# Kernel tuning notes

Measured on AMD Instinct MI355X. Metric: run time of the kernel, lower is better.

The kernel has to match this reference:

```python
import jax, jax.numpy as jnp
import numpy as np

D_MODEL = 1024
NUM_HEADS = 16
D_HEAD = D_MODEL // NUM_HEADS


def setup_inputs() -> dict:
    key = jax.random.key(0)
    ks = jax.random.split(key, 7)
    B, S = 2, 2048
    scale = 1.0 / np.sqrt(D_MODEL)
    return {
        "x": jax.random.normal(ks[0], (B, S, D_MODEL), dtype=jnp.float32),
        "attn_weights": jnp.zeros((1,), dtype=jnp.float32),  # unused in original forward
        "Wq": jax.random.normal(ks[1], (D_MODEL, D_MODEL), dtype=jnp.float32) * scale,
        "Wk": jax.random.normal(ks[2], (D_MODEL, D_MODEL), dtype=jnp.float32) * scale,
        "Wv": jax.random.normal(ks[3], (D_MODEL, D_MODEL), dtype=jnp.float32) * scale,
        "Wp": jax.random.normal(ks[4], (D_MODEL, D_MODEL), dtype=jnp.float32) * scale,
        "bp": jnp.zeros((D_MODEL,), dtype=jnp.float32),
    }


def reference(x, attn_weights, Wq, Wk, Wv, Wp, bp):
    B, S, D = x.shape
    H, Dh = NUM_HEADS, D_HEAD
    # torch Linear: y = x @ W.T  (weights stored [out, in])
    q = (x @ Wq.T).reshape(B, S, H, Dh).transpose(0, 2, 1, 3)  # [B,H,S,Dh]
    k = (x @ Wk.T).reshape(B, S, H, Dh).transpose(0, 2, 1, 3)
    v = (x @ Wv.T).reshape(B, S, H, Dh).transpose(0, 2, 1, 3)
    # NOTE: original module applies NO 1/sqrt(d) scaling
    scores = jnp.einsum("bhqd,bhkd->bhqk", q, k)
    weights = jax.nn.softmax(scores, axis=-1)  # dropout is inference no-op
    out = jnp.einsum("bhqk,bhkd->bhqd", weights, v)
    out = out.transpose(0, 2, 1, 3).reshape(B, S, D)
    return out @ Wp.T + bp
```

## Files before the change

### kernel.cpp

```cpp
#include <hip/hip_runtime.h>
#include <hip/hip_bf16.h>

#define D_MODEL 1024
#define NUM_HEADS 16
#define D_HEAD 64
#define BATCH 2
#define SEQ 2048
#define TOKENS (BATCH * SEQ)

typedef __attribute__((ext_vector_type(8))) short bf16x8;
typedef __attribute__((ext_vector_type(4))) float f32x4;
typedef __attribute__((ext_vector_type(2))) unsigned int uint2v;

typedef __attribute__((address_space(1))) const unsigned int as1_uint;
typedef __attribute__((address_space(3))) unsigned int as3_uint;

#define LOG2E 1.44269504088896340736f

static __device__ __forceinline__ unsigned short f2bf(float f) {
    unsigned int u = __builtin_bit_cast(unsigned int, f);
    u += 0x7fffu + ((u >> 16) & 1u);
    return (unsigned short)(u >> 16);
}

static __device__ __forceinline__ unsigned int pk2bf(float a, float b) {
    __hip_bfloat162 h = __float22bfloat162_rn(float2{a, b});
    unsigned int u;
    __builtin_memcpy(&u, &h, 4);
    return u;
}

static __device__ __forceinline__ float fast_exp2(float x) {
    return __builtin_amdgcn_exp2f(x);
}

__global__ __launch_bounds__(256) void convert_bf16(
    const float* __restrict__ x,  const float* __restrict__ Wq,
    const float* __restrict__ Wk, const float* __restrict__ Wv,
    const float* __restrict__ Wp,
    unsigned short* __restrict__ xb,  unsigned short* __restrict__ Wqb,
    unsigned short* __restrict__ Wkb, unsigned short* __restrict__ Wvb,
    unsigned short* __restrict__ Wpb)
{
    int v = blockIdx.x * 256 + threadIdx.x;
    const float* s;
    unsigned short* d;
    int off;
    if (v < (1 << 20)) { s = x; d = xb; off = v; }
    else {
        int u = v - (1 << 20);
        int w = u >> 18;
        off = u & ((1 << 18) - 1);
        s = (w == 0) ? Wq : (w == 1) ? Wk : (w == 2) ? Wv : Wp;
        d = (w == 0) ? Wqb : (w == 1) ? Wkb : (w == 2) ? Wvb : Wpb;
    }
    float4 f = ((const float4*)s)[off];
    ushort4 o = { f2bf(f.x), f2bf(f.y), f2bf(f.z), f2bf(f.w) };
    ((ushort4*)d)[off] = o;
}

__global__ __launch_bounds__(512, 4) void qkv_gemm(
    const unsigned short* __restrict__ xb,
    const unsigned short* __restrict__ Wqb, const unsigned short* __restrict__ Wkb,
    const unsigned short* __restrict__ Wvb,
    unsigned short* __restrict__ Q, unsigned short* __restrict__ Kb,
    unsigned short* __restrict__ Vt)
{
    const int m0 = blockIdx.x * 128;
    const int n0 = blockIdx.y * 64;

    __shared__ __attribute__((aligned(16))) unsigned short sm[40960];

    const int t = threadIdx.x;
    const int wave = t >> 6, lane = t & 63;
    const int wm = (wave & 1) * 64, wn = (wave >> 1) * 16;
    const int l15 = lane & 15, quad = lane >> 4;
    const int sw = l15 & 7;

    const unsigned short* Wz[3] = { Wqb, Wkb, Wvb };

    f32x4 acc[3][4];
#pragma unroll
    for (int z = 0; z < 3; z++)
#pragma unroll
        for (int i = 0; i < 4; i++) acc[z][i] = (f32x4)0.f;

    auto stage = [&](int k0, int buf) {
#pragma unroll
        for (int i = 0; i < 2; i++) {
            int fbase = wave * 64 + i * 512;
            int f = fbase + lane;
            int row = f >> 3, cp = f & 7;
            int c = cp ^ (row & 7);
            __builtin_amdgcn_global_load_lds(
                (as1_uint*)&xb[(size_t)(m0 + row) * D_MODEL + k0 + c * 8],
                (as3_uint*)&sm[buf * 20480 + fbase * 8], 16, 0, 0);
        }
        {
            int row = t >> 3, cp = t & 7;
            int c = cp ^ (row & 7);
            int fbase = wave * 64;
#pragma unroll
            for (int z = 0; z < 3; z++)
                __builtin_amdgcn_global_load_lds(
                    (as1_uint*)&Wz[z][(size_t)(n0 + row) * D_MODEL + k0 + c * 8],
                    (as3_uint*)&sm[buf * 20480 + 8192 + z * 4096 + fbase * 8],
                    16, 0, 0);
        }
    };

    stage(0, 0);
    __syncthreads();

    int cur = 0;
    for (int k0 = 0; k0 < D_MODEL; k0 += 64) {
        if (k0 + 64 < D_MODEL) stage(k0 + 64, cur ^ 1);

        const unsigned short* lA = &sm[cur * 20480];
#pragma unroll
        for (int kk = 0; kk < 2; kk++) {
            const int cc = ((kk * 4 + quad) ^ sw) * 8;
            bf16x8 a[4];
#pragma unroll
            for (int mt = 0; mt < 4; mt++)
                a[mt] = *(const bf16x8*)&lA[(wm + mt * 16 + l15) * 64 + cc];
#pragma unroll
            for (int z = 0; z < 3; z++) {
                const unsigned short* lB = &sm[cur * 20480 + 8192 + z * 4096];
                bf16x8 b = *(const bf16x8*)&lB[(wn + l15) * 64 + cc];
#pragma unroll
                for (int mt = 0; mt < 4; mt++)
                    acc[z][mt] = __builtin_amdgcn_mfma_f32_16x16x32_bf16(
                        a[mt], b, acc[z][mt], 0, 0, 0);
            }
        }
        __syncthreads();
        cur ^= 1;
    }

#pragma unroll
    for (int mt = 0; mt < 4; mt++)
#pragma unroll
        for (int r = 0; r < 4; r++) {
            int row = m0 + wm + mt * 16 + quad * 4 + r;
            int col = n0 + wn + l15;
            Q[(size_t)row * D_MODEL + col]  = f2bf(acc[0][mt][r] * LOG2E);
            Kb[(size_t)row * D_MODEL + col] = f2bf(acc[1][mt][r]);
        }
    {
        const int b = m0 >> 11;
        const int srow = (m0 & 2047) + wm + quad * 4;
        const int h = n0 >> 6;
        const int dh = wn + l15;
#pragma unroll
        for (int mt = 0; mt < 4; mt++) {
            ushort4 pk = { f2bf(acc[2][mt][0]), f2bf(acc[2][mt][1]),
                           f2bf(acc[2][mt][2]), f2bf(acc[2][mt][3]) };
            *(ushort4*)&Vt[(size_t)((b * 16 + h) * 64 + dh) * SEQ + srow + mt * 16] = pk;
        }
    }
}

__global__ __launch_bounds__(512, 4) void attn(
    const unsigned short* __restrict__ Q, const unsigned short* __restrict__ K,
    const unsigned short* __restrict__ Vt, unsigned short* __restrict__ O)
{
    const int q0 = blockIdx.x * 128;
    const int bh = blockIdx.y;
    const int b = bh >> 4, h = bh & 15;
    const size_t base = (size_t)b * SEQ * D_MODEL + (size_t)h * D_HEAD;
    const size_t baseV = (size_t)bh * D_HEAD * SEQ;

    __shared__ __attribute__((aligned(16))) char smem[40960];
    unsigned short* lK0 = (unsigned short*)&smem[0];
    unsigned short* lV0 = (unsigned short*)&smem[16384];

    const int t = threadIdx.x;
    const int wave = t >> 6, lane = t & 63;
    const int l15 = lane & 15, quad = lane >> 4;
    const int wq = wave & 3;
    const int sh = wave >> 2;
    const int qw = q0 + wq * 32;
    const int sbase = sh * (SEQ / 2);

    unsigned short* lK  = lK0 + sh * 4096;
    unsigned short* lVt = lV0 + sh * 4096;

    bf16x8 ones;
#pragma unroll
    for (int i = 0; i < 8; i++) ones[i] = (short)0x3F80;

    bf16x8 bq[2][2];
#pragma unroll
    for (int mq = 0; mq < 2; mq++)
#pragma unroll
        for (int kk = 0; kk < 2; kk++)
            bq[mq][kk] = *(const bf16x8*)&Q[base +
                (size_t)(qw + mq * 16 + l15) * D_MODEL + kk * 32 + quad * 8];

    const int tl = t & 255;
    const int r0 = tl >> 3, c0 = tl & 7;
    const int cs = (c0 ^ (r0 & 7)) * 8;
    const unsigned short* gK0 = &K[base + (size_t)(sbase + r0) * D_MODEL + c0 * 8];
    const unsigned short* gK1 = &K[base + (size_t)(sbase + r0 + 32) * D_MODEL + c0 * 8];
    const unsigned short* gV0 = &Vt[baseV + (size_t)r0 * SEQ + sbase + c0 * 8];
    const unsigned short* gV1 = &Vt[baseV + (size_t)(r0 + 32) * SEQ + sbase + c0 * 8];

    const int sw = l15 & 7;

    f32x4 o_acc[2][4];
#pragma unroll
    for (int i = 0; i < 2; i++)
#pragma unroll
        for (int j = 0; j < 4; j++) o_acc[i][j] = (f32x4)0.f;
    f32x4 o_l[2];
#pragma unroll
    for (int i = 0; i < 2; i++) o_l[i] = (f32x4)0.f;

    uint4 rK0 = *(const uint4*)gK0;
    uint4 rK1 = *(const uint4*)gK1;
    uint4 rV0 = *(const uint4*)gV0;
    uint4 rV1 = *(const uint4*)gV1;

    for (int s0 = 0; s0 < SEQ / 2; s0 += 64) {
        __syncthreads();
        *(uint4*)&lK[r0 * 64 + cs]        = rK0;
        *(uint4*)&lK[(r0 + 32) * 64 + cs] = rK1;
        *(uint4*)&lVt[r0 * 64 + cs]        = rV0;
        *(uint4*)&lVt[(r0 + 32) * 64 + cs] = rV1;
        __syncthreads();

        int sn = (s0 + 64 < SEQ / 2) ? s0 + 64 : 0;
        rK0 = *(const uint4*)(gK0 + (size_t)sn * D_MODEL);
        rK1 = *(const uint4*)(gK1 + (size_t)sn * D_MODEL);
        rV0 = *(const uint4*)(gV0 + sn);
        rV1 = *(const uint4*)(gV1 + sn);

        f32x4 st[4][2];
#pragma unroll
        for (int mt = 0; mt < 4; mt++)
#pragma unroll
            for (int mq = 0; mq < 2; mq++) st[mt][mq] = (f32x4)0.f;
#pragma unroll
        for (int kk = 0; kk < 2; kk++) {
            const int cc = ((kk * 4 + quad) ^ sw) * 8;
#pragma unroll
            for (int mt = 0; mt < 4; mt++) {
                bf16x8 ak = *(const bf16x8*)&lK[(mt * 16 + l15) * 64 + cc];
#pragma unroll
                for (int mq = 0; mq < 2; mq++)
                    st[mt][mq] = __builtin_amdgcn_mfma_f32_16x16x32_bf16(
                        ak, bq[mq][kk], st[mt][mq], 0, 0, 0);
            }
        }

#pragma unroll
        for (int mq = 0; mq < 2; mq++)
#pragma unroll
            for (int mt = 0; mt < 4; mt++)
#pragma unroll
                for (int r = 0; r < 4; r++)
                    st[mt][mq][r] = fast_exp2(st[mt][mq][r]);

        bf16x8 pa[2][2];
#pragma unroll
        for (int mq = 0; mq < 2; mq++)
#pragma unroll
            for (int kk = 0; kk < 2; kk++) {
                unsigned int cw[4];
#pragma unroll
                for (int j = 0; j < 2; j++) {
                    unsigned int w0 = pk2bf(st[2 * kk][mq][2 * j],
                                            st[2 * kk][mq][2 * j + 1]);
                    unsigned int w1 = pk2bf(st[2 * kk + 1][mq][2 * j],
                                            st[2 * kk + 1][mq][2 * j + 1]);
                    uint2v uv = __builtin_amdgcn_permlane32_swap(w0, w1, false, false);
                    uint2v f  = __builtin_amdgcn_permlane16_swap(uv[0], uv[1], false, false);
                    cw[j]     = f[0];
                    cw[2 + j] = f[1];
                }
                union { unsigned int w[4]; bf16x8 v; } u;
                u.w[0] = cw[0]; u.w[1] = cw[1]; u.w[2] = cw[2]; u.w[3] = cw[3];
                pa[mq][kk] = u.v;
            }

#pragma unroll
        for (int kk = 0; kk < 2; kk++) {
            const int cc = ((kk * 4 + quad) ^ sw) * 8;
            bf16x8 bv[4];
#pragma unroll
            for (int nt = 0; nt < 4; nt++)
                bv[nt] = *(const bf16x8*)&lVt[(nt * 16 + l15) * 64 + cc];
#pragma unroll
            for (int mq = 0; mq < 2; mq++) {
#pragma unroll
                for (int nt = 0; nt < 4; nt++)
                    o_acc[mq][nt] = __builtin_amdgcn_mfma_f32_16x16x32_bf16(
                        pa[mq][kk], bv[nt], o_acc[mq][nt], 0, 0, 0);
                o_l[mq] = __builtin_amdgcn_mfma_f32_16x16x32_bf16(
                    pa[mq][kk], ones, o_l[mq], 0, 0, 0);
            }
        }
    }

    float* sO = (float*)&smem[0];
    float* sL = (float*)&smem[36864];
    __syncthreads();
    if (sh == 1) {
#pragma unroll
        for (int mq = 0; mq < 2; mq++) {
#pragma unroll
            for (int r = 0; r < 4; r++)
                sL[wq * 32 + mq * 16 + quad * 4 + r] = o_l[mq][r];
#pragma unroll
            for (int nt = 0; nt < 4; nt++)
#pragma unroll
                for (int r = 0; r < 4; r++)
                    sO[(wq * 32 + mq * 16 + quad * 4 + r) * 68 + nt * 16 + l15] =
                        o_acc[mq][nt][r];
        }
    }
    __syncthreads();
    if (sh == 0) {
#pragma unroll
        for (int mq = 0; mq < 2; mq++) {
            float inv[4];
#pragma unroll
            for (int r = 0; r < 4; r++)
                inv[r] = 1.f / (o_l[mq][r] + sL[wq * 32 + mq * 16 + quad * 4 + r]);
#pragma unroll
            for (int nt = 0; nt < 4; nt++)
#pragma unroll
                for (int r = 0; r < 4; r++) {
                    int row = qw + mq * 16 + quad * 4 + r;
                    float v = o_acc[mq][nt][r] +
                              sO[(wq * 32 + mq * 16 + quad * 4 + r) * 68 + nt * 16 + l15];
                    O[base + (size_t)row * D_MODEL + nt * 16 + l15] = f2bf(v * inv[r]);
                }
        }
    }
}

__global__ __launch_bounds__(512, 4) void proj_gemm(
    const unsigned short* __restrict__ A, const unsigned short* __restrict__ W,
    const float* __restrict__ bias, float* __restrict__ out)
{
    const int m0 = blockIdx.x * 128;
    const int n0 = blockIdx.y * 64;

    __shared__ __attribute__((aligned(16))) unsigned short sm[24576];

    const int t = threadIdx.x;
    const int wave = t >> 6, lane = t & 63;
    const int wm = (wave & 1) * 64, wn = (wave >> 1) * 16;
    const int l15 = lane & 15, quad = lane >> 4;
    const int sw = l15 & 7;

    f32x4 acc[4];
#pragma unroll
    for (int i = 0; i < 4; i++) acc[i] = (f32x4)0.f;

    auto stage = [&](int k0, int buf) {
#pragma unroll
        for (int i = 0; i < 2; i++) {
            int fbase = wave * 64 + i * 512;
            int f = fbase + lane;
            int row = f >> 3, cp = f & 7;
            int c = cp ^ (row & 7);
            __builtin_amdgcn_global_load_lds(
                (as1_uint*)&A[(size_t)(m0 + row) * D_MODEL + k0 + c * 8],
                (as3_uint*)&sm[buf * 12288 + fbase * 8], 16, 0, 0);
        }
        {
            int row = t >> 3, cp = t & 7;
            int c = cp ^ (row & 7);
            int fbase = wave * 64;
            __builtin_amdgcn_global_load_lds(
                (as1_uint*)&W[(size_t)(n0 + row) * D_MODEL + k0 + c * 8],
                (as3_uint*)&sm[buf * 12288 + 8192 + fbase * 8], 16, 0, 0);
        }
    };

    stage(0, 0);
    __syncthreads();

    int cur = 0;
    for (int k0 = 0; k0 < D_MODEL; k0 += 64) {
        if (k0 + 64 < D_MODEL) stage(k0 + 64, cur ^ 1);

        const unsigned short* lA = &sm[cur * 12288];
        const unsigned short* lB = &sm[cur * 12288 + 8192];
#pragma unroll
        for (int kk = 0; kk < 2; kk++) {
            const int cc = ((kk * 4 + quad) ^ sw) * 8;
            bf16x8 a[4];
#pragma unroll
            for (int mt = 0; mt < 4; mt++)
                a[mt] = *(const bf16x8*)&lA[(wm + mt * 16 + l15) * 64 + cc];
            bf16x8 b = *(const bf16x8*)&lB[(wn + l15) * 64 + cc];
#pragma unroll
            for (int mt = 0; mt < 4; mt++)
                acc[mt] = __builtin_amdgcn_mfma_f32_16x16x32_bf16(
                    a[mt], b, acc[mt], 0, 0, 0);
        }
        __syncthreads();
        cur ^= 1;
    }

    const int col = n0 + wn + l15;
    const float bc = bias[col];
#pragma unroll
    for (int mt = 0; mt < 4; mt++)
#pragma unroll
        for (int r = 0; r < 4; r++) {
            int row = m0 + wm + mt * 16 + quad * 4 + r;
            out[(size_t)row * D_MODEL + col] = acc[mt][r] + bc;
        }
}

extern "C" void kernel_launch(void* const* d_in, const int* in_sizes, int n_in,
                              void* d_out, int out_size, void* d_ws, size_t ws_size,
                              hipStream_t stream)
{
    const float* x  = (const float*)d_in[0];
    const float* Wq = (const float*)d_in[2];
    const float* Wk = (const float*)d_in[3];
    const float* Wv = (const float*)d_in[4];
    const float* Wp = (const float*)d_in[5];
    const float* bp = (const float*)d_in[6];
    float* out = (float*)d_out;

    unsigned short* Q   = (unsigned short*)d_ws;
    unsigned short* K   = Q   + (size_t)TOKENS * D_MODEL;
    unsigned short* Vt  = K   + (size_t)TOKENS * D_MODEL;
    unsigned short* O   = Vt  + (size_t)TOKENS * D_MODEL;
    unsigned short* xb  = O   + (size_t)TOKENS * D_MODEL;
    unsigned short* Wqb = xb  + (size_t)TOKENS * D_MODEL;
    unsigned short* Wkb = Wqb + (size_t)D_MODEL * D_MODEL;
    unsigned short* Wvb = Wkb + (size_t)D_MODEL * D_MODEL;
    unsigned short* Wpb = Wvb + (size_t)D_MODEL * D_MODEL;

    convert_bf16<<<8192, 256, 0, stream>>>(x, Wq, Wk, Wv, Wp,
                                           xb, Wqb, Wkb, Wvb, Wpb);
    qkv_gemm<<<dim3(TOKENS / 128, D_MODEL / 64), 512, 0, stream>>>(
        xb, Wqb, Wkb, Wvb, Q, K, Vt);
    attn<<<dim3(SEQ / 128, BATCH * NUM_HEADS), 512, 0, stream>>>(Q, K, Vt, O);
    proj_gemm<<<dim3(TOKENS / 128, D_MODEL / 64), 512, 0, stream>>>(O, Wpb, bp, out);
}
```

Before: 170.1 us.

## Double-buffer K/V tiles in LDS using direct global-to-LDS loads

The attention kernel stops staging K and Vt tiles through registers and copies them straight from global memory into LDS with global_load_lds. Two LDS buffers let the next tile load while the current one is computed, so only one barrier per iteration remains. The cost is LDS growing from 40 KB to 64 KB per block, which can cut the number of resident blocks per CU below the launch-bounds target. Correctness also relies on the async LDS writes being complete before the end-of-iteration barrier.

```diff
diff --git a/kernel.cpp b/kernel.cpp
--- a/kernel.cpp
+++ b/kernel.cpp
@@ -171,9 +171,8 @@
     const size_t base = (size_t)b * SEQ * D_MODEL + (size_t)h * D_HEAD;
     const size_t baseV = (size_t)bh * D_HEAD * SEQ;
 
-    __shared__ __attribute__((aligned(16))) char smem[40960];
-    unsigned short* lK0 = (unsigned short*)&smem[0];
-    unsigned short* lV0 = (unsigned short*)&smem[16384];
+    __shared__ __attribute__((aligned(16))) char smem[65536];
+    unsigned short* lds = (unsigned short*)smem;
 
     const int t = threadIdx.x;
     const int wave = t >> 6, lane = t & 63;
@@ -183,9 +182,6 @@
     const int qw = q0 + wq * 32;
     const int sbase = sh * (SEQ / 2);
 
-    unsigned short* lK  = lK0 + sh * 4096;
-    unsigned short* lVt = lV0 + sh * 4096;
-
     bf16x8 ones;
 #pragma unroll
     for (int i = 0; i < 8; i++) ones[i] = (short)0x3F80;
@@ -199,14 +195,22 @@
                 (size_t)(qw + mq * 16 + l15) * D_MODEL + kk * 32 + quad * 8];
 
     const int tl = t & 255;
-    const int r0 = tl >> 3, c0 = tl & 7;
-    const int cs = (c0 ^ (r0 & 7)) * 8;
-    const unsigned short* gK0 = &K[base + (size_t)(sbase + r0) * D_MODEL + c0 * 8];
-    const unsigned short* gK1 = &K[base + (size_t)(sbase + r0 + 32) * D_MODEL + c0 * 8];
-    const unsigned short* gV0 = &Vt[baseV + (size_t)r0 * SEQ + sbase + c0 * 8];
-    const unsigned short* gV1 = &Vt[baseV + (size_t)(r0 + 32) * SEQ + sbase + c0 * 8];
-
     const int sw = l15 & 7;
+
+    auto stage = [&](int soff, int buf) {
+#pragma unroll
+        for (int i = 0; i < 2; i++) {
+            int f = tl + i * 256;
+            int row = f >> 3;
+            int c = (f & 7) ^ (row & 7);
+            __builtin_amdgcn_global_load_lds(
+                (as1_uint*)&K[base + (size_t)(sbase + soff + row) * D_MODEL + c * 8],
+                (as3_uint*)&lds[buf * 16384 + sh * 4096 + f * 8], 16, 0, 0);
+            __builtin_amdgcn_global_load_lds(
+                (as1_uint*)&Vt[baseV + (size_t)row * SEQ + sbase + soff + c * 8],
+                (as3_uint*)&lds[8192 + buf * 16384 + sh * 4096 + f * 8], 16, 0, 0);
+        }
+    };
 
     f32x4 o_acc[2][4];
 #pragma unroll
@@ -217,24 +221,15 @@
 #pragma unroll
     for (int i = 0; i < 2; i++) o_l[i] = (f32x4)0.f;
 
-    uint4 rK0 = *(const uint4*)gK0;
-    uint4 rK1 = *(const uint4*)gK1;
-    uint4 rV0 = *(const uint4*)gV0;
-    uint4 rV1 = *(const uint4*)gV1;
-
+    stage(0, 0);
+    __syncthreads();
+
+    int cur = 0;
     for (int s0 = 0; s0 < SEQ / 2; s0 += 64) {
-        __syncthreads();
-        *(uint4*)&lK[r0 * 64 + cs]        = rK0;
-        *(uint4*)&lK[(r0 + 32) * 64 + cs] = rK1;
-        *(uint4*)&lVt[r0 * 64 + cs]        = rV0;
-        *(uint4*)&lVt[(r0 + 32) * 64 + cs] = rV1;
-        __syncthreads();
-
-        int sn = (s0 + 64 < SEQ / 2) ? s0 + 64 : 0;
-        rK0 = *(const uint4*)(gK0 + (size_t)sn * D_MODEL);
-        rK1 = *(const uint4*)(gK1 + (size_t)sn * D_MODEL);
-        rV0 = *(const uint4*)(gV0 + sn);
-        rV1 = *(const uint4*)(gV1 + sn);
+        if (s0 + 64 < SEQ / 2) stage(s0 + 64, cur ^ 1);
+
+        const unsigned short* lK  = lds + cur * 16384 + sh * 4096;
+        const unsigned short* lVt = lds + 8192 + cur * 16384 + sh * 4096;
 
         f32x4 st[4][2];
 #pragma unroll
@@ -279,9 +274,9 @@
                     cw[j]     = f[0];
                     cw[2 + j] = f[1];
                 }
-                union { unsigned int w[4]; bf16x8 v; } u;
-                u.w[0] = cw[0]; u.w[1] = cw[1]; u.w[2] = cw[2]; u.w[3] = cw[3];
-                pa[mq][kk] = u.v;
+                union { unsigned int w[4]; bf16x8 v; } uu;
+                uu.w[0] = cw[0]; uu.w[1] = cw[1]; uu.w[2] = cw[2]; uu.w[3] = cw[3];
+                pa[mq][kk] = uu.v;
             }
 
 #pragma unroll
@@ -301,11 +296,12 @@
                     pa[mq][kk], ones, o_l[mq], 0, 0, 0);
             }
         }
+        __syncthreads();
+        cur ^= 1;
     }
 
     float* sO = (float*)&smem[0];
     float* sL = (float*)&smem[36864];
-    __syncthreads();
     if (sh == 1) {
 #pragma unroll
         for (int mq = 0; mq < 2; mq++) {
```

Result: no change. 172.2 us (+1.2%).
